# Performance work log

Measured on AMD Instinct MI355X. Metric: run time of the kernel, lower is better.

Reference implementation:

```python
import jax, jax.numpy as jnp
import numpy as np

B, C, H, W = 2, 256, 48, 48
NH = 4          # heads (and SE ratio)
DK = C // NH    # 64


def conv1x1(x, w, b):
    # x: [B,Cin,H,W], w: [Cout,Cin], b: [Cout]
    return jnp.einsum('oc,bchw->bohw', w, x) + b[None, :, None, None]


def rtrans(q_in, k_in, v_in, qw, qb, kw, kb, vw, vb):
    b, c, h_, w_ = q_in.shape
    n = h_ * w_
    q = conv1x1(q_in, qw, qb).reshape(b, NH, DK, n).transpose(0, 1, 3, 2)  # [B,h,N,dk]
    k = conv1x1(k_in, kw, kb).reshape(b, NH, DK, n)                         # [B,h,dk,N]
    v = conv1x1(v_in, vw, vb).reshape(b, NH, DK, n)                         # [B,h,dk,N]
    scores = jnp.einsum('bhnd,bhdm->bhnm', q, k) / jnp.sqrt(jnp.asarray(DK, q.dtype))
    attn = jax.nn.softmax(scores, axis=-1)                                  # [B,h,N,N]
    out = jnp.einsum('bhdn,bhnm->bhdm', v, attn)                            # [B,h,dk,N]
    return out.reshape(b, c, h_, w_)


def setup_inputs() -> dict:
    key = jax.random.key(0)
    ks = jax.random.split(key, 16)
    s = 0.02
    d = {
        'x': jax.random.normal(ks[0], (B, C, H, W), jnp.float32),
        'y': jax.random.normal(ks[1], (B, C, H, W), jnp.float32),
        # RScaling: fc1 Conv2d(2C, C//ratio, 1), fc2 Conv2d(C//ratio, 2C, 1); ratio=NH
        'sc_fc1_w': jax.random.normal(ks[2], (C // NH, 2 * C), jnp.float32) * s,
        'sc_fc1_b': jnp.zeros((C // NH,), jnp.float32),
        'sc_fc2_w': jax.random.normal(ks[3], (2 * C, C // NH), jnp.float32) * s,
        'sc_fc2_b': jnp.zeros((2 * C,), jnp.float32),
        # RTrans 1
        't1_qw': jax.random.normal(ks[4], (C, C), jnp.float32) * s,
        't1_qb': jnp.zeros((C,), jnp.float32),
        't1_kw': jax.random.normal(ks[5], (C, C), jnp.float32) * s,
        't1_kb': jnp.zeros((C,), jnp.float32),
        't1_vw': jax.random.normal(ks[6], (C, C), jnp.float32) * s,
        't1_vb': jnp.zeros((C,), jnp.float32),
        # RTrans 2 (ST=True)
        't2_qw': jax.random.normal(ks[7], (C, C), jnp.float32) * s,
        't2_qb': jnp.zeros((C,), jnp.float32),
        't2_kw': jax.random.normal(ks[8], (C, C), jnp.float32) * s,
        't2_kb': jnp.zeros((C,), jnp.float32),
        't2_vw': jax.random.normal(ks[9], (C, C), jnp.float32) * s,
        't2_vb': jnp.zeros((C,), jnp.float32),
        # RGating: Conv2d(2C, 2, 1)
        'gate_w': jax.random.normal(ks[10], (2, 2 * C), jnp.float32) * s,
        'gate_b': jnp.zeros((2,), jnp.float32),
    }
    return d


def reference(x, y, sc_fc1_w, sc_fc1_b, sc_fc2_w, sc_fc2_b,
              t1_qw, t1_qb, t1_kw, t1_kb, t1_vw, t1_vb,
              t2_qw, t2_qb, t2_kw, t2_kb, t2_vw, t2_vb,
              gate_w, gate_b):
    c = x.shape[1]
    # --- RScaling (SE squeeze-excite on concatenated streams) ---
    cat = jnp.concatenate([x, y], axis=1)                       # [B,2C,H,W]
    pooled = cat.mean(axis=(2, 3), keepdims=True)               # [B,2C,1,1]
    f = conv1x1(jax.nn.relu(conv1x1(pooled, sc_fc1_w, sc_fc1_b)), sc_fc2_w, sc_fc2_b)
    g = jax.nn.sigmoid(f)                                       # [B,2C,1,1]
    x = x * g[:, :c] + x
    y = y * g[:, c:] + y
    # --- RTrans 1: x = attn(q=x, k=y, v=y) ---
    x = rtrans(x, y, y, t1_qw, t1_qb, t1_kw, t1_kb, t1_vw, t1_vb)
    # --- RTrans 2 (ST): y = attn(q=y, k=x_new, v=x_new) ---
    y = rtrans(y, x, x, t2_qw, t2_qb, t2_kw, t2_kb, t2_vw, t2_vb)
    # --- RGating ---
    gate = jax.nn.sigmoid(conv1x1(jnp.concatenate([x, y], axis=1), gate_w, gate_b))  # [B,2,H,W]
    x = x * gate[:, :1] + x
    y = y * gate[:, 1:] + y
    return (x, y)
```

## Files before the change

### kernel.cpp

```cpp
#include <hip/hip_runtime.h>
#include <hip/hip_bf16.h>
#include <math.h>

typedef __hip_bfloat16 bf16;
typedef unsigned short u16;
typedef __attribute__((ext_vector_type(8))) short short8;
typedef __attribute__((ext_vector_type(4))) float f32x4;

#define BB  2
#define CC  256
#define NHH 4
#define DKK 64
#define NN  2304
#define NT  36
#define NT2 18
#define MFMA16(a,b,c) __builtin_amdgcn_mfma_f32_16x16x32_bf16(a, b, c, 0, 0, 0)

__device__ __forceinline__ float u2f(u16 u){ return __uint_as_float(((unsigned)u) << 16); }
__device__ __forceinline__ u16 f2u(float f){
    unsigned u = __float_as_uint(f);
    unsigned r = u + 0x7FFFu + ((u >> 16) & 1u);
    return (u16)(r >> 16);
}

__device__ __forceinline__ float ldv(const void* p, size_t i, int bf){
    return bf ? u2f(((const u16*)p)[i]) : ((const float*)p)[i];
}
__device__ __forceinline__ void stv(void* p, size_t i, float v, int bf){
    if (bf) ((u16*)p)[i] = f2u(v);
    else    ((float*)p)[i] = v;
}
__device__ __forceinline__ short8 ldw8(const void* p, size_t i, int bf){
    if (bf) return *(const short8*)((const u16*)p + i);
    const float* f = (const float*)p + i;
    short8 r;
    #pragma unroll
    for (int k = 0; k < 8; k++) r[k] = (short)f2u(f[k]);
    return r;
}

__global__ void detect_kernel(const void* __restrict__ x, int* __restrict__ flg){
    const u16* u = (const u16*)x;
    int t = threadIdx.x;
    bool ok = true;
    for (int i = 0; i < 8; i++){
        u16 v = u[t*8 + i];
        int e = (v >> 7) & 0xFF;
        ok = ok && (((v & 0x7FFF) == 0) || (e >= 96 && e <= 143));
    }
    unsigned long long b = __ballot(ok);
    if (t == 0) *flg = (b == 0xFFFFFFFFFFFFFFFFull) ? 1 : 0;
}

__global__ void pool_kernel(const void* __restrict__ x, const void* __restrict__ y,
                            const int* __restrict__ flg, float* __restrict__ pooled){
    int bf = *flg;
    int bid = blockIdx.x;
    int b = bid >> 9, cc = bid & 511;
    const void* src = (cc < CC) ? x : y;
    size_t base = ((size_t)b*CC + (cc & 255))*NN;
    float s = 0.f;
    for (int i = threadIdx.x; i < NN; i += 256) s += ldv(src, base + i, bf);
    __shared__ float red[4];
    for (int off = 32; off; off >>= 1) s += __shfl_down(s, off, 64);
    if ((threadIdx.x & 63) == 0) red[threadIdx.x >> 6] = s;
    __syncthreads();
    if (threadIdx.x == 0)
        pooled[bid] = (red[0]+red[1]+red[2]+red[3]) * (1.0f/(float)NN);
}

__global__ void se_kernel(const float* __restrict__ pooled,
                          const void* __restrict__ w1, const void* __restrict__ b1,
                          const void* __restrict__ w2, const void* __restrict__ b2v,
                          const int* __restrict__ flg, float* __restrict__ gse){
    int bf = *flg;
    int b = blockIdx.x;
    __shared__ float ps[512];
    __shared__ float f1[64];
    int t = threadIdx.x;
    ps[t]     = pooled[b*512 + t];
    ps[t+256] = pooled[b*512 + 256 + t];
    __syncthreads();
    if (t < 64){
        float a = ldv(b1, t, bf);
        for (int c = 0; c < 512; c++) a += ldv(w1, t*512 + c, bf) * ps[c];
        f1[t] = fmaxf(a, 0.f);
    }
    __syncthreads();
    for (int o = t; o < 512; o += 256){
        float a = ldv(b2v, o, bf);
        for (int j = 0; j < 64; j++) a += ldv(w2, o*64 + j, bf) * f1[j];
        gse[b*512 + o] = 1.f + 1.f/(1.f + __expf(-a));
    }
}

__global__ void transpose2_kernel(const void* __restrict__ x, const void* __restrict__ y,
                                  const float* __restrict__ gse, const int* __restrict__ flg,
                                  u16* __restrict__ xsT, u16* __restrict__ ysT){
    int bf = *flg;
    int z = blockIdx.z;
    int b = z >> 1, which = z & 1;
    const void* src = which ? y : x;
    const float* gs = gse + b*512 + (which ? 256 : 0);
    u16* dst = which ? ysT : xsT;
    int ct = blockIdx.y, nt = blockIdx.x;
    int t = threadIdx.x;
    int nl = t & 63, cq = t >> 6;
    #pragma unroll
    for (int i = 0; i < 16; i++){
        int c = ct*64 + cq*16 + i;
        float v = ldv(src, ((size_t)b*CC + c)*NN + nt*64 + nl, bf) * gs[c];
        dst[((size_t)b*NN + nt*64 + nl)*CC + c] = f2u(v);
    }
}

__launch_bounds__(256)
__global__ void conv3_mfma(const u16* __restrict__ Xq, const u16* __restrict__ Xkv,
                           const void* __restrict__ wq, const void* __restrict__ bq,
                           const void* __restrict__ wk, const void* __restrict__ bk,
                           const void* __restrict__ wv, const void* __restrict__ bv_,
                           const int* __restrict__ flg,
                           u16* __restrict__ QT, u16* __restrict__ KT, u16* __restrict__ Vb){
    int bf = *flg;
    int z = blockIdx.z;
    int b = z / 3, op = z % 3;
    const u16* X = (op == 0) ? Xq : Xkv;
    const void* W    = (op == 0) ? wq : (op == 1) ? wk : wv;
    const void* bias = (op == 0) ? bq : (op == 1) ? bk : bv_;
    u16* Y = (op == 0) ? QT : (op == 1) ? KT : Vb;
    int transT = (op < 2);
    int ot = blockIdx.y, nt = blockIdx.x;
    int lane = threadIdx.x & 63, wv_ = threadIdx.x >> 6;
    int c15 = lane & 15, quad = lane >> 4;
    const u16* Xb = X + ((size_t)b*NN + nt*64)*CC;
    int oa = ot*64 + wv_*16 + c15;
    f32x4 zf = {0.f,0.f,0.f,0.f};
    f32x4 acc[4] = {zf,zf,zf,zf};
    #pragma unroll
    for (int kc = 0; kc < CC; kc += 32){
        short8 aw = ldw8(W, (size_t)oa*CC + kc + quad*8, bf);
        #pragma unroll
        for (int j = 0; j < 4; j++){
            short8 bx = *(const short8*)(Xb + (size_t)(j*16 + c15)*CC + kc + quad*8);
            acc[j] = MFMA16(aw, bx, acc[j]);
        }
    }
    int od = ot*64 + wv_*16 + quad*4;
    float bvr[4];
    #pragma unroll
    for (int r = 0; r < 4; r++) bvr[r] = ldv(bias, od + r, bf);
    #pragma unroll
    for (int j = 0; j < 4; j++){
        int n = nt*64 + j*16 + c15;
        #pragma unroll
        for (int r = 0; r < 4; r++){
            int o = od + r;
            float val = acc[j][r] + bvr[r];
            size_t idx = transT
              ? (((size_t)(b*NHH + (o >> 6))*NN + n)*DKK + (o & 63))
              : (((size_t)b*CC + o)*NN + n);
            Y[idx] = f2u(val);
        }
    }
}

__launch_bounds__(512)
__global__ void attn_stats_mfma(const u16* __restrict__ QT, const u16* __restrict__ KT,
                                float* __restrict__ M, float* __restrict__ Li){
    int bh = blockIdx.y, ntile = blockIdx.x;
    int tid = threadIdx.x;
    int lane = tid & 63, wv5 = tid >> 6;
    int g = wv5 >> 2, wv = wv5 & 3;
    int c15 = lane & 15, quad = lane >> 4;
    const u16* Qb = QT + (size_t)bh*NN*DKK;
    const u16* Kb = KT + (size_t)bh*NN*DKK;
    size_t qo = (size_t)(ntile*64 + wv*16 + c15)*DKK + quad*8;
    short8 a0 = *(const short8*)(Qb + qo);
    short8 a1 = *(const short8*)(Qb + qo + 32);
    float Mr[4] = {-3e38f,-3e38f,-3e38f,-3e38f};
    float Lr[4] = {0.f,0.f,0.f,0.f};
    f32x4 z = {0.f,0.f,0.f,0.f};
    for (int it = 0; it < NT2; it++){
        int mt = g*NT2 + it;
        f32x4 s[4];
        #pragma unroll
        for (int j = 0; j < 4; j++){
            size_t ko = (size_t)(mt*64 + j*16 + c15)*DKK + quad*8;
            short8 b0 = *(const short8*)(Kb + ko);
            short8 b1 = *(const short8*)(Kb + ko + 32);
            f32x4 t = MFMA16(a0, b0, z);
            s[j]     = MFMA16(a1, b1, t);
        }
        #pragma unroll
        for (int r = 0; r < 4; r++){
            float v0 = 0.125f*s[0][r], v1 = 0.125f*s[1][r];
            float v2 = 0.125f*s[2][r], v3 = 0.125f*s[3][r];
            float mx = fmaxf(fmaxf(v0,v1), fmaxf(v2,v3));
            #pragma unroll
            for (int d = 1; d < 16; d <<= 1) mx = fmaxf(mx, __shfl_xor(mx, d, 16));
            float nM = fmaxf(Mr[r], mx);
            float es = __expf(v0-nM)+__expf(v1-nM)+__expf(v2-nM)+__expf(v3-nM);
            #pragma unroll
            for (int d = 1; d < 16; d <<= 1) es += __shfl_xor(es, d, 16);
            Lr[r] = Lr[r]*__expf(Mr[r]-nM) + es;
            Mr[r] = nM;
        }
    }
    __shared__ float Ms[2][64], Ls[2][64];
    if (c15 == 0){
        #pragma unroll
        for (int r = 0; r < 4; r++){
            int nl = wv*16 + quad*4 + r;
            Ms[g][nl] = Mr[r];
            Ls[g][nl] = Lr[r];
        }
    }
    __syncthreads();
    if (g == 0 && c15 == 0){
        #pragma unroll
        for (int r = 0; r < 4; r++){
            int nl = wv*16 + quad*4 + r;
            float m0 = Ms[0][nl], m1 = Ms[1][nl];
            float mm = fmaxf(m0, m1);
            float ll = Ls[0][nl]*__expf(m0-mm) + Ls[1][nl]*__expf(m1-mm);
            int n = ntile*64 + nl;
            M[(size_t)bh*NN + n]  = mm;
            Li[(size_t)bh*NN + n] = 1.f/ll;
        }
    }
}

__launch_bounds__(512)
__global__ void attn_out_mfma(const u16* __restrict__ QT, const u16* __restrict__ KT,
                              const u16* __restrict__ V, const float* __restrict__ M,
                              const float* __restrict__ Li, const int* __restrict__ flg,
                              void* __restrict__ O, size_t ooff, u16* __restrict__ OT){
    int bf = *flg;
    int bh = blockIdx.y, mtile = blockIdx.x;
    int tid = threadIdx.x;
    int lane = tid & 63, wv5 = tid >> 6;
    int g = wv5 >> 2, wv = wv5 & 3;
    int c15 = lane & 15, quad = lane >> 4;
    const u16* Qb = QT + (size_t)bh*NN*DKK;
    const u16* Kb = KT + (size_t)bh*NN*DKK;
    const u16* Vb = V + (size_t)bh*DKK*NN;
    const float* Mp = M + (size_t)bh*NN;
    const float* Lp = Li + (size_t)bh*NN;
    __shared__ __align__(16) u16 wT[2][2][64][72];
    __shared__ __align__(16) float osum[64][65];
    short8 kb0[4], kb1[4];
    #pragma unroll
    for (int j = 0; j < 4; j++){
        size_t ko = (size_t)(mtile*64 + j*16 + c15)*DKK + quad*8;
        kb0[j] = *(const short8*)(Kb + ko);
        kb1[j] = *(const short8*)(Kb + ko + 32);
    }
    f32x4 z = {0.f,0.f,0.f,0.f};
    f32x4 o4[4] = {z,z,z,z};
    for (int it = 0; it < NT2; it++){
        int nt = g*NT2 + it;
        int p = it & 1;
        size_t qo = (size_t)(nt*64 + wv*16 + c15)*DKK + quad*8;
        short8 a0 = *(const short8*)(Qb + qo);
        short8 a1 = *(const short8*)(Qb + qo + 32);
        f32x4 s[4];
        #pragma unroll
        for (int j = 0; j < 4; j++){
            f32x4 t = MFMA16(a0, kb0[j], z);
            s[j]    = MFMA16(a1, kb1[j], t);
        }
        int nb = nt*64 + wv*16 + quad*4;
        float Mr[4], iL[4];
        #pragma unroll
        for (int r = 0; r < 4; r++){ Mr[r] = Mp[nb+r]; iL[r] = Lp[nb+r]; }
        size_t vo = (size_t)(wv*16 + c15)*NN + nt*64 + quad*8;
        short8 av0 = *(const short8*)(Vb + vo);
        short8 av1 = *(const short8*)(Vb + vo + 32);
        #pragma unroll
        for (int j = 0; j < 4; j++){
            ushort4 pk;
            pk.x = f2u(__expf(0.125f*s[j][0] - Mr[0]) * iL[0]);
            pk.y = f2u(__expf(0.125f*s[j][1] - Mr[1]) * iL[1]);
            pk.z = f2u(__expf(0.125f*s[j][2] - Mr[2]) * iL[2]);
            pk.w = f2u(__expf(0.125f*s[j][3] - Mr[3]) * iL[3]);
            *(ushort4*)&wT[g][p][j*16 + c15][wv*16 + quad*4] = pk;
        }
        __syncthreads();
        #pragma unroll
        for (int j = 0; j < 4; j++){
            short8 b0 = *(const short8*)&wT[g][p][j*16 + c15][quad*8];
            short8 b1 = *(const short8*)&wT[g][p][j*16 + c15][32 + quad*8];
            o4[j] = MFMA16(av0, b0, o4[j]);
            o4[j] = MFMA16(av1, b1, o4[j]);
        }
    }
    if (g == 1){
        #pragma unroll
        for (int j = 0; j < 4; j++)
            #pragma unroll
            for (int r = 0; r < 4; r++)
                osum[wv*16 + quad*4 + r][j*16 + c15] = o4[j][r];
    }
    __syncthreads();
    if (g == 0){
        int brow = bh >> 2, head = bh & 3;
        #pragma unroll
        for (int j = 0; j < 4; j++){
            int m = mtile*64 + j*16 + c15;
            #pragma unroll
            for (int r = 0; r < 4; r++){
                int d = wv*16 + quad*4 + r;
                float val = o4[j][r] + osum[d][j*16 + c15];
                stv(O, ooff + ((size_t)brow*CC + head*DKK + d)*NN + m, val, bf);
                if (OT) OT[((size_t)brow*NN + m)*CC + head*DKK + d] = f2u(val);
            }
        }
    }
}

__global__ void gate_part_kernel(const void* __restrict__ out, const void* __restrict__ gw,
                                 const int* __restrict__ flg, float* __restrict__ gpart){
    int bf = *flg;
    const size_t SZ = (size_t)BB*CC*NN;
    int b = blockIdx.z, g = blockIdx.y;
    int nb = blockIdx.x*64;
    int t = threadIdx.x;
    int nl = t & 63, sub = t >> 6;
    __shared__ float r0[4][64], r1[4][64];
    float a0 = 0.f, a1 = 0.f;
    int cbase = g*128 + sub*32;
    for (int i = 0; i < 32; i++){
        int cc = cbase + i;
        size_t idx = (cc < 256 ? ((size_t)b*CC + cc)*NN
                               : SZ + ((size_t)b*CC + (cc-256))*NN) + nb + nl;
        float v = ldv(out, idx, bf);
        a0 += ldv(gw, cc, bf)*v;
        a1 += ldv(gw, 512 + cc, bf)*v;
    }
    r0[sub][nl] = a0; r1[sub][nl] = a1;
    __syncthreads();
    if (t < 64){
        float s0 = r0[0][t]+r0[1][t]+r0[2][t]+r0[3][t];
        float s1 = r1[0][t]+r1[1][t]+r1[2][t]+r1[3][t];
        int n = nb + t;
        gpart[(((size_t)b*4 + g)*2 + 0)*NN + n] = s0;
        gpart[(((size_t)b*4 + g)*2 + 1)*NN + n] = s1;
    }
}

__global__ void gate_combine_kernel(const float* __restrict__ gpart, const void* __restrict__ gb,
                                    const int* __restrict__ flg, float* __restrict__ gates){
    int bf = *flg;
    int idx = blockIdx.x*256 + threadIdx.x;
    if (idx >= BB*NN) return;
    int b = idx / NN, n = idx % NN;
    float s0 = ldv(gb, 0, bf), s1 = ldv(gb, 1, bf);
    #pragma unroll
    for (int g = 0; g < 4; g++){
        s0 += gpart[(((size_t)b*4 + g)*2 + 0)*NN + n];
        s1 += gpart[(((size_t)b*4 + g)*2 + 1)*NN + n];
    }
    gates[((size_t)b*2 + 0)*NN + n] = 1.f + 1.f/(1.f + __expf(-s0));
    gates[((size_t)b*2 + 1)*NN + n] = 1.f + 1.f/(1.f + __expf(-s1));
}

__global__ void rescale_kernel(const float* __restrict__ gates, const int* __restrict__ flg,
                               void* __restrict__ out){
    int bf = *flg;
    const size_t SZ = (size_t)BB*CC*NN;
    const size_t nq = (2*SZ) >> 2;
    for (size_t u = (size_t)blockIdx.x*256 + threadIdx.x; u < nq; u += (size_t)gridDim.x*256){
        size_t flat = u*4;
        int half = (int)(flat / SZ);
        size_t rem = flat % SZ;
        int b = (int)(rem / ((size_t)CC*NN));
        int n = (int)(rem % NN);
        const float* gp = gates + ((size_t)b*2 + half)*NN + n;
        #pragma unroll
        for (int k = 0; k < 4; k++)
            stv(out, flat + k, ldv(out, flat + k, bf) * gp[k], bf);
    }
}

extern "C" void kernel_launch(void* const* d_in, const int* in_sizes, int n_in,
                              void* d_out, int out_size, void* d_ws, size_t ws_size,
                              hipStream_t stream){
    (void)in_sizes; (void)n_in; (void)out_size; (void)ws_size;
    const void* x    = d_in[0];
    const void* y    = d_in[1];
    const void* sc1w = d_in[2];
    const void* sc1b = d_in[3];
    const void* sc2w = d_in[4];
    const void* sc2b = d_in[5];
    const void *t1qw = d_in[6],  *t1qb = d_in[7];
    const void *t1kw = d_in[8],  *t1kb = d_in[9];
    const void *t1vw = d_in[10], *t1vb = d_in[11];
    const void *t2qw = d_in[12], *t2qb = d_in[13];
    const void *t2kw = d_in[14], *t2kb = d_in[15];
    const void *t2vw = d_in[16], *t2vb = d_in[17];
    const void *gw   = d_in[18], *gb   = d_in[19];

    const size_t SZ = (size_t)BB*CC*NN;
    char* wsb = (char*)d_ws;
    int*   flg    = (int*)wsb;
    float* pooled = (float*)(wsb + 16);
    float* gse    = pooled + 1024;
    float* Mb     = gse + 1024;
    float* Lb     = Mb + (size_t)BB*NHH*NN;
    float* gpart  = Lb + (size_t)BB*NHH*NN;
    float* gates  = gpart + (size_t)BB*4*2*NN;
    u16* xsT = (u16*)(gates + (size_t)BB*2*NN);
    u16* ysT = xsT + SZ;
    u16* QT  = ysT + SZ;
    u16* KT  = QT + SZ;
    u16* Vb  = KT + SZ;

    dim3 tg2(NT, 4, BB*2);
    dim3 cg3(NT, 4, BB*3);
    dim3 ag(NT, BB*NHH);
    dim3 gg(NT, 4, BB);

    detect_kernel<<<1, 64, 0, stream>>>(x, flg);
    pool_kernel<<<1024, 256, 0, stream>>>(x, y, flg, pooled);
    se_kernel<<<BB, 256, 0, stream>>>(pooled, sc1w, sc1b, sc2w, sc2b, flg, gse);

    transpose2_kernel<<<tg2, 256, 0, stream>>>(x, y, gse, flg, xsT, ysT);

    conv3_mfma<<<cg3, 256, 0, stream>>>(xsT, ysT, t1qw, t1qb, t1kw, t1kb, t1vw, t1vb,
                                        flg, QT, KT, Vb);
    attn_stats_mfma<<<ag, 512, 0, stream>>>(QT, KT, Mb, Lb);
    attn_out_mfma<<<ag, 512, 0, stream>>>(QT, KT, Vb, Mb, Lb, flg, d_out, 0, xsT);

    conv3_mfma<<<cg3, 256, 0, stream>>>(ysT, xsT, t2qw, t2qb, t2kw, t2kb, t2vw, t2vb,
                                        flg, QT, KT, Vb);
    attn_stats_mfma<<<ag, 512, 0, stream>>>(QT, KT, Mb, Lb);
    attn_out_mfma<<<ag, 512, 0, stream>>>(QT, KT, Vb, Mb, Lb, flg, d_out, SZ, (u16*)nullptr);

    gate_part_kernel<<<gg, 256, 0, stream>>>(d_out, gw, flg, gpart);
    gate_combine_kernel<<<18, 256, 0, stream>>>(gpart, gb, flg, gates);
    rescale_kernel<<<1024, 256, 0, stream>>>(gates, flg, d_out);
}
```

Baseline: 474.0 us.

## Split softmax stats over key chunks, defer lane reductions, fold scale into K

The softmax-statistics kernel now splits the key dimension into four chunks across a third grid dimension, launching 256-thread blocks with more blocks in total. A new combine kernel merges the partial max and sum values. Each lane keeps its own running max and sum, and the cross-lane shuffle reduction is done once at the end instead of on every tile. The 1/sqrt(dk) scale is folded into the K projection output, which removes per-element multiplies in both attention kernels. The cost is an extra kernel launch and workspace traffic for the partial statistics.

Measured after the change: 434.9 us. -8.2%, faster.

```diff
diff --git a/kernel.cpp b/kernel.cpp
--- a/kernel.cpp
+++ b/kernel.cpp
@@ -14,6 +14,8 @@
 #define NN  2304
 #define NT  36
 #define NT2 18
+#define MS  4
+#define NTM 9
 #define MFMA16(a,b,c) __builtin_amdgcn_mfma_f32_16x16x32_bf16(a, b, c, 0, 0, 0)
 
 __device__ __forceinline__ float u2f(u16 u){ return __uint_as_float(((unsigned)u) << 16); }
@@ -129,6 +131,7 @@
     const void* bias = (op == 0) ? bq : (op == 1) ? bk : bv_;
     u16* Y = (op == 0) ? QT : (op == 1) ? KT : Vb;
     int transT = (op < 2);
+    float oscale = (op == 1) ? 0.125f : 1.0f;
     int ot = blockIdx.y, nt = blockIdx.x;
     int lane = threadIdx.x & 63, wv_ = threadIdx.x >> 6;
     int c15 = lane & 15, quad = lane >> 4;
@@ -155,7 +158,7 @@
         #pragma unroll
         for (int r = 0; r < 4; r++){
             int o = od + r;
-            float val = acc[j][r] + bvr[r];
+            float val = (acc[j][r] + bvr[r]) * oscale;
             size_t idx = transT
               ? (((size_t)(b*NHH + (o >> 6))*NN + n)*DKK + (o & 63))
               : (((size_t)b*CC + o)*NN + n);
@@ -164,24 +167,22 @@
     }
 }
 
-__launch_bounds__(512)
+__launch_bounds__(256)
 __global__ void attn_stats_mfma(const u16* __restrict__ QT, const u16* __restrict__ KT,
-                                float* __restrict__ M, float* __restrict__ Li){
-    int bh = blockIdx.y, ntile = blockIdx.x;
-    int tid = threadIdx.x;
-    int lane = tid & 63, wv5 = tid >> 6;
-    int g = wv5 >> 2, wv = wv5 & 3;
+                                float* __restrict__ gM, float* __restrict__ gL){
+    int bh = blockIdx.y, ntile = blockIdx.x, ms = blockIdx.z;
+    int lane = threadIdx.x & 63, wv = threadIdx.x >> 6;
     int c15 = lane & 15, quad = lane >> 4;
     const u16* Qb = QT + (size_t)bh*NN*DKK;
     const u16* Kb = KT + (size_t)bh*NN*DKK;
     size_t qo = (size_t)(ntile*64 + wv*16 + c15)*DKK + quad*8;
     short8 a0 = *(const short8*)(Qb + qo);
     short8 a1 = *(const short8*)(Qb + qo + 32);
-    float Mr[4] = {-3e38f,-3e38f,-3e38f,-3e38f};
-    float Lr[4] = {0.f,0.f,0.f,0.f};
+    float ml[4] = {-3e38f,-3e38f,-3e38f,-3e38f};
+    float ll[4] = {0.f,0.f,0.f,0.f};
     f32x4 z = {0.f,0.f,0.f,0.f};
-    for (int it = 0; it < NT2; it++){
-        int mt = g*NT2 + it;
+    for (int it = 0; it < NTM; it++){
+        int mt = ms*NTM + it;
         f32x4 s[4];
         #pragma unroll
         for (int j = 0; j < 4; j++){
@@ -193,41 +194,51 @@
         }
         #pragma unroll
         for (int r = 0; r < 4; r++){
-            float v0 = 0.125f*s[0][r], v1 = 0.125f*s[1][r];
-            float v2 = 0.125f*s[2][r], v3 = 0.125f*s[3][r];
-            float mx = fmaxf(fmaxf(v0,v1), fmaxf(v2,v3));
-            #pragma unroll
-            for (int d = 1; d < 16; d <<= 1) mx = fmaxf(mx, __shfl_xor(mx, d, 16));
-            float nM = fmaxf(Mr[r], mx);
-            float es = __expf(v0-nM)+__expf(v1-nM)+__expf(v2-nM)+__expf(v3-nM);
-            #pragma unroll
-            for (int d = 1; d < 16; d <<= 1) es += __shfl_xor(es, d, 16);
-            Lr[r] = Lr[r]*__expf(Mr[r]-nM) + es;
-            Mr[r] = nM;
-        }
-    }
-    __shared__ float Ms[2][64], Ls[2][64];
+            float v0 = s[0][r], v1 = s[1][r], v2 = s[2][r], v3 = s[3][r];
+            float vmax = fmaxf(fmaxf(v0,v1), fmaxf(v2,v3));
+            float mn = fmaxf(ml[r], vmax);
+            float es = __expf(v0-mn)+__expf(v1-mn)+__expf(v2-mn)+__expf(v3-mn);
+            ll[r] = ll[r]*__expf(ml[r]-mn) + es;
+            ml[r] = mn;
+        }
+    }
+    #pragma unroll
+    for (int d = 1; d < 16; d <<= 1){
+        #pragma unroll
+        for (int r = 0; r < 4; r++){
+            float mo = __shfl_xor(ml[r], d, 16);
+            float lo = __shfl_xor(ll[r], d, 16);
+            float mn = fmaxf(ml[r], mo);
+            ll[r] = ll[r]*__expf(ml[r]-mn) + lo*__expf(mo-mn);
+            ml[r] = mn;
+        }
+    }
     if (c15 == 0){
         #pragma unroll
         for (int r = 0; r < 4; r++){
-            int nl = wv*16 + quad*4 + r;
-            Ms[g][nl] = Mr[r];
-            Ls[g][nl] = Lr[r];
-        }
-    }
-    __syncthreads();
-    if (g == 0 && c15 == 0){
-        #pragma unroll
-        for (int r = 0; r < 4; r++){
-            int nl = wv*16 + quad*4 + r;
-            float m0 = Ms[0][nl], m1 = Ms[1][nl];
-            float mm = fmaxf(m0, m1);
-            float ll = Ls[0][nl]*__expf(m0-mm) + Ls[1][nl]*__expf(m1-mm);
-            int n = ntile*64 + nl;
-            M[(size_t)bh*NN + n]  = mm;
-            Li[(size_t)bh*NN + n] = 1.f/ll;
-        }
-    }
+            int n = ntile*64 + wv*16 + quad*4 + r;
+            size_t o = ((size_t)ms*BB*NHH + bh)*NN + n;
+            gM[o] = ml[r];
+            gL[o] = ll[r];
+        }
+    }
+}
+
+__global__ void stats_combine(const float* __restrict__ gM, const float* __restrict__ gL,
+                              float* __restrict__ M, float* __restrict__ Li){
+    int idx = blockIdx.x*256 + threadIdx.x;
+    if (idx >= BB*NHH*NN) return;
+    float mm = -3e38f, ll = 0.f;
+    #pragma unroll
+    for (int ms = 0; ms < MS; ms++){
+        float m = gM[(size_t)ms*BB*NHH*NN + idx];
+        float l = gL[(size_t)ms*BB*NHH*NN + idx];
+        float mn = fmaxf(mm, m);
+        ll = ll*__expf(mm-mn) + l*__expf(m-mn);
+        mm = mn;
+    }
+    M[idx]  = mm;
+    Li[idx] = 1.f/ll;
 }
 
 __launch_bounds__(512)
@@ -279,10 +290,10 @@
         #pragma unroll
         for (int j = 0; j < 4; j++){
             ushort4 pk;
-            pk.x = f2u(__expf(0.125f*s[j][0] - Mr[0]) * iL[0]);
-            pk.y = f2u(__expf(0.125f*s[j][1] - Mr[1]) * iL[1]);
-            pk.z = f2u(__expf(0.125f*s[j][2] - Mr[2]) * iL[2]);
-            pk.w = f2u(__expf(0.125f*s[j][3] - Mr[3]) * iL[3]);
+            pk.x = f2u(__expf(s[j][0] - Mr[0]) * iL[0]);
+            pk.y = f2u(__expf(s[j][1] - Mr[1]) * iL[1]);
+            pk.z = f2u(__expf(s[j][2] - Mr[2]) * iL[2]);
+            pk.w = f2u(__expf(s[j][3] - Mr[3]) * iL[3]);
             *(ushort4*)&wT[g][p][j*16 + c15][wv*16 + quad*4] = pk;
         }
         __syncthreads();
@@ -401,13 +412,16 @@
     const void *gw   = d_in[18], *gb   = d_in[19];
 
     const size_t SZ = (size_t)BB*CC*NN;
+    const size_t BHN = (size_t)BB*NHH*NN;
     char* wsb = (char*)d_ws;
     int*   flg    = (int*)wsb;
     float* pooled = (float*)(wsb + 16);
     float* gse    = pooled + 1024;
     float* Mb     = gse + 1024;
-    float* Lb     = Mb + (size_t)BB*NHH*NN;
-    float* gpart  = Lb + (size_t)BB*NHH*NN;
+    float* Lb     = Mb + BHN;
+    float* gM     = Lb + BHN;
+    float* gL     = gM + MS*BHN;
+    float* gpart  = gL + MS*BHN;
     float* gates  = gpart + (size_t)BB*4*2*NN;
     u16* xsT = (u16*)(gates + (size_t)BB*2*NN);
     u16* ysT = xsT + SZ;
@@ -417,6 +431,7 @@
 
     dim3 tg2(NT, 4, BB*2);
     dim3 cg3(NT, 4, BB*3);
+    dim3 sg(NT, BB*NHH, MS);
     dim3 ag(NT, BB*NHH);
     dim3 gg(NT, 4, BB);
 
@@ -428,12 +443,14 @@
 
     conv3_mfma<<<cg3, 256, 0, stream>>>(xsT, ysT, t1qw, t1qb, t1kw, t1kb, t1vw, t1vb,
                                         flg, QT, KT, Vb);
-    attn_stats_mfma<<<ag, 512, 0, stream>>>(QT, KT, Mb, Lb);
+    attn_stats_mfma<<<sg, 256, 0, stream>>>(QT, KT, gM, gL);
+    stats_combine<<<72, 256, 0, stream>>>(gM, gL, Mb, Lb);
     attn_out_mfma<<<ag, 512, 0, stream>>>(QT, KT, Vb, Mb, Lb, flg, d_out, 0, xsT);
 
     conv3_mfma<<<cg3, 256, 0, stream>>>(ysT, xsT, t2qw, t2qb, t2kw, t2kb, t2vw, t2vb,
                                         flg, QT, KT, Vb);
-    attn_stats_mfma<<<ag, 512, 0, stream>>>(QT, KT, Mb, Lb);
+    attn_stats_mfma<<<sg, 256, 0, stream>>>(QT, KT, gM, gL);
+    stats_combine<<<72, 256, 0, stream>>>(gM, gL, Mb, Lb);
     attn_out_mfma<<<ag, 512, 0, stream>>>(QT, KT, Vb, Mb, Lb, flg, d_out, SZ, (u16*)nullptr);
 
     gate_part_kernel<<<gg, 256, 0, stream>>>(d_out, gw, flg, gpart);
```
